# Optimization experiments

Measured on AMD Instinct MI355X. Metric: run time of the kernel, lower is better.

The kernel has to match this reference:

```python
import jax, jax.numpy as jnp
import numpy as np

NUM_GRAPHS = 256
NODES_PER_GRAPH = 64
K = 24
HID = 128

elu = jax.nn.elu


def _knn_edge_conv(x, Wc, bc):
    # x: [B*N, D]. Recompute kNN graph per graph, edge MLP, max-aggregate.
    B, N = NUM_GRAPHS, NODES_PER_GRAPH
    xg = x.reshape(B, N, -1)                       # [B, N, D]
    sq = jnp.sum(xg * xg, axis=-1)                 # [B, N]
    # squared euclidean distances within each graph: [B, N, N]
    d = sq[:, :, None] + sq[:, None, :] - 2.0 * jnp.einsum('bnd,bmd->bnm', xg, xg)
    _, idx = jax.lax.top_k(-d, K)                  # [B, N, K] nearest (incl. self)
    xj = jax.vmap(lambda g, i: g[i])(xg, idx)      # [B, N, K, D] neighbor gather
    xi = xg[:, :, None, :]                         # [B, N, 1, D]
    e = jnp.concatenate([jnp.broadcast_to(xi, xj.shape), xj - xi], axis=-1)  # [B,N,K,2D]
    m = elu(jnp.einsum('bnkf,fh->bnkh', e, Wc) + bc)
    out = jnp.max(m, axis=2)                       # max aggregation over K neighbors
    return out.reshape(B * N, -1)


def setup_inputs() -> dict:
    key = jax.random.key(0)
    ks = jax.random.split(key, 16)
    Ntot = NUM_GRAPHS * NODES_PER_GRAPH

    def w(k, fan_in, fan_out):
        return jax.random.normal(k, (fan_in, fan_out), jnp.float32) / np.sqrt(fan_in)

    return {
        'x_pf': jax.random.normal(ks[0], (Ntot, 15), jnp.float32),
        'batch_pf': jnp.repeat(jnp.arange(NUM_GRAPHS, dtype=jnp.int64 if jax.config.jax_enable_x64 else jnp.int32), NODES_PER_GRAPH),
        'W1': w(ks[1], 15, HID),  'b1': jnp.zeros((HID,), jnp.float32),
        'W2': w(ks[2], HID, HID), 'b2': jnp.zeros((HID,), jnp.float32),
        'Wc': w(ks[3], 2 * HID, HID), 'bc': jnp.zeros((HID,), jnp.float32),
        'Wo1': w(ks[4], HID, 64), 'bo1': jnp.zeros((64,), jnp.float32),
        'Wo2': w(ks[5], 64, 32),  'bo2': jnp.zeros((32,), jnp.float32),
        'Wo3': w(ks[6], 32, 32),  'bo3': jnp.zeros((32,), jnp.float32),
        'Wo4': w(ks[7], 32, 8),   'bo4': jnp.zeros((8,), jnp.float32),
    }


def reference(x_pf, batch_pf, W1, b1, W2, b2, Wc, bc, Wo1, bo1, Wo2, bo2, Wo3, bo3, Wo4, bo4):
    # pf_encode: Linear(15,128)+ELU+Linear(128,128)+ELU
    h = elu(elu(x_pf @ W1 + b1) @ W2 + b2)
    f1 = _knn_edge_conv(h, Wc, bc)
    f2 = _knn_edge_conv(f1, Wc, bc)
    f3 = _knn_edge_conv(f2, Wc, bc)
    # global_add_pool over nodes per graph
    pooled = jax.ops.segment_sum(f3, batch_pf, num_segments=NUM_GRAPHS)  # [B, 128]
    o = elu(pooled @ Wo1 + bo1)
    o = elu(o @ Wo2 + bo2)
    o = elu(o @ Wo3 + bo3)
    out = o @ Wo4 + bo4  # [B, 8]
    return (out, batch_pf)
```

## Files before the change

### kernel.cpp

```cpp
#include <hip/hip_runtime.h>
#include <hip/hip_bf16.h>
#include <math.h>

#define NG  256
#define NN  64
#define KK  24
#define HID 128
#define KP  136
#define FP  132
#define DP  68
#define FRAG 512
#define SLAB (8*4*2*FRAG)
#define HSLAB (8*4*FRAG)
#define IMG_BYTES (3*SLAB*2)

typedef __attribute__((ext_vector_type(8)))  short bf16x8;
typedef __attribute__((ext_vector_type(4)))  float f32x4;

__device__ __forceinline__ float elu1(float x){ return x > 0.f ? x : (expf(x)-1.f); }

__device__ __forceinline__ short bf_t(float x){ return (short)(__float_as_uint(x) >> 16); }
__device__ __forceinline__ float bf_u(short s){ return __uint_as_float(((unsigned)(unsigned short)s) << 16); }

extern "C" __global__ void prep_kernel(const float* __restrict__ W2,
                                       const float* __restrict__ Wc,
                                       short* __restrict__ img)
{
    int t = blockIdx.x * 256 + threadIdx.x;
    if (t >= 3*8*4*64) return;
    const int lane = t & 63;
    const int ks   = (t >> 6) & 3;
    const int tn   = (t >> 8) & 7;
    const int s    = t >> 11;
    const int n     = tn*16 + (lane & 15);
    const int kbase = ks*32 + (lane >> 4)*8;
    bf16x8 hv, lv;
    #pragma unroll
    for (int j = 0; j < 8; ++j){
        const int k = kbase + j;
        float w = (s == 0) ? W2[k*HID + n]
                : (s == 1) ? Wc[k*HID + n]
                           : Wc[(k + HID)*HID + n];
        short h = bf_t(w);
        hv[j] = h;
        lv[j] = bf_t(w - bf_u(h));
    }
    short* dst = img + s*SLAB + ((tn*4 + ks)*2)*FRAG + lane*8;
    *(bf16x8*)(dst)        = hv;
    *(bf16x8*)(dst + FRAG) = lv;
}

__device__ __forceinline__ void stage_copy(const short* __restrict__ src,
                                           short* __restrict__ slab, int tid)
{
    const uint4* s = (const uint4*)src;
    uint4* d = (uint4*)slab;
    #pragma unroll
    for (int i = 0; i < 4; ++i) d[tid + i*1024] = s[tid + i*1024];
}

__device__ __forceinline__ void stage_build(const float* __restrict__ Wg, int rowoff,
                                            short* __restrict__ slab, int tid)
{
    for (int i = tid; i < 8*4*64; i += 1024){
        const int lane2 = i & 63;
        const int ks    = (i >> 6) & 3;
        const int tn    = (i >> 8) & 7;
        const int n     = tn*16 + (lane2 & 15);
        const int kbase = ks*32 + (lane2 >> 4)*8;
        bf16x8 hv, lv;
        #pragma unroll
        for (int j = 0; j < 8; ++j){
            float w = Wg[(rowoff + kbase + j)*HID + n];
            short h = bf_t(w);
            hv[j] = h;
            lv[j] = bf_t(w - bf_u(h));
        }
        short* dst = slab + ((tn*4 + ks)*2)*FRAG + lane2*8;
        *(bf16x8*)(dst)        = hv;
        *(bf16x8*)(dst + FRAG) = lv;
    }
}

__device__ __forceinline__ void stage_hi_uv(const short* __restrict__ img,
                                            short* __restrict__ uv, int tid)
{
    const uint4* s = (const uint4*)img;
    uint4* d = (uint4*)uv;
    #pragma unroll
    for (int k = 0; k < 4; ++k){
        const int idx    = tid + k*1024;
        const int sl     = idx >> 11;
        const int within = idx & 2047;
        const int f      = within >> 6;
        const int w      = within & 63;
        d[idx] = s[(1 + sl)*4096 + f*128 + w];
    }
}

__device__ __forceinline__ void build_hi_uv(const float* __restrict__ Wc,
                                            short* __restrict__ uv, int tid)
{
    #pragma unroll
    for (int k = 0; k < 4; ++k){
        const int idx    = tid + k*1024;
        const int sl     = idx >> 11;
        const int within = idx & 2047;
        const int f      = within >> 6;
        const int lane2  = within & 63;
        const int tn = f >> 2, ks = f & 3;
        const int n     = tn*16 + (lane2 & 15);
        const int kbase = ks*32 + (lane2 >> 4)*8;
        const int rowoff = sl ? HID : 0;
        bf16x8 hv;
        #pragma unroll
        for (int j = 0; j < 8; ++j) hv[j] = bf_t(Wc[(rowoff + kbase + j)*HID + n]);
        *(bf16x8*)(uv + (size_t)idx*8) = hv;
    }
}

__device__ __forceinline__ void gemm16x2(const short* __restrict__ fbhi,
                                         const short* __restrict__ fblo,
                                         const short* __restrict__ slab,
                                         int tm, int tn0, int tn1, int lane,
                                         f32x4& c0, f32x4& c1)
{
    const int arow = tm*16 + (lane & 15);
    const int ko   = (lane >> 4) * 8;
    #pragma unroll 2
    for (int ks = 0; ks < 4; ++ks){
        bf16x8 ah = *(const bf16x8*)(fbhi + arow*KP + ks*32 + ko);
        bf16x8 al = *(const bf16x8*)(fblo + arow*KP + ks*32 + ko);
        const short* p0 = slab + ((tn0*4 + ks)*2)*FRAG + lane*8;
        const short* p1 = slab + ((tn1*4 + ks)*2)*FRAG + lane*8;
        bf16x8 bh0 = *(const bf16x8*)(p0);
        bf16x8 bl0 = *(const bf16x8*)(p0 + FRAG);
        bf16x8 bh1 = *(const bf16x8*)(p1);
        bf16x8 bl1 = *(const bf16x8*)(p1 + FRAG);
        c0 = __builtin_amdgcn_mfma_f32_16x16x32_bf16(ah, bh0, c0, 0,0,0);
        c0 = __builtin_amdgcn_mfma_f32_16x16x32_bf16(ah, bl0, c0, 0,0,0);
        c0 = __builtin_amdgcn_mfma_f32_16x16x32_bf16(al, bh0, c0, 0,0,0);
        c1 = __builtin_amdgcn_mfma_f32_16x16x32_bf16(ah, bh1, c1, 0,0,0);
        c1 = __builtin_amdgcn_mfma_f32_16x16x32_bf16(ah, bl1, c1, 0,0,0);
        c1 = __builtin_amdgcn_mfma_f32_16x16x32_bf16(al, bh1, c1, 0,0,0);
    }
}

__device__ __forceinline__ void gemm_uv(const short* __restrict__ fbhi,
                                        const short* __restrict__ fblo,
                                        const short* __restrict__ uhi,
                                        const short* __restrict__ vhi,
                                        int tm, int tn0, int tn1, int lane,
                                        f32x4& uA, f32x4& uB, f32x4& vA, f32x4& vB)
{
    const int arow = tm*16 + (lane & 15);
    const int ko   = (lane >> 4) * 8;
    #pragma unroll 2
    for (int ks = 0; ks < 4; ++ks){
        bf16x8 ah = *(const bf16x8*)(fbhi + arow*KP + ks*32 + ko);
        bf16x8 al = *(const bf16x8*)(fblo + arow*KP + ks*32 + ko);
        const int f0 = (tn0*4 + ks)*FRAG + lane*8;
        const int f1 = (tn1*4 + ks)*FRAG + lane*8;
        bf16x8 bu0 = *(const bf16x8*)(uhi + f0);
        bf16x8 bu1 = *(const bf16x8*)(uhi + f1);
        bf16x8 bv0 = *(const bf16x8*)(vhi + f0);
        bf16x8 bv1 = *(const bf16x8*)(vhi + f1);
        uA = __builtin_amdgcn_mfma_f32_16x16x32_bf16(ah, bu0, uA, 0,0,0);
        uA = __builtin_amdgcn_mfma_f32_16x16x32_bf16(al, bu0, uA, 0,0,0);
        uB = __builtin_amdgcn_mfma_f32_16x16x32_bf16(ah, bu1, uB, 0,0,0);
        uB = __builtin_amdgcn_mfma_f32_16x16x32_bf16(al, bu1, uB, 0,0,0);
        vA = __builtin_amdgcn_mfma_f32_16x16x32_bf16(ah, bv0, vA, 0,0,0);
        vA = __builtin_amdgcn_mfma_f32_16x16x32_bf16(al, bv0, vA, 0,0,0);
        vB = __builtin_amdgcn_mfma_f32_16x16x32_bf16(ah, bv1, vB, 0,0,0);
        vB = __builtin_amdgcn_mfma_f32_16x16x32_bf16(al, bv1, vB, 0,0,0);
    }
}

extern "C" __global__ void __launch_bounds__(1024)
dgcnn_kernel(const float* __restrict__ x_pf,
             const float* __restrict__ W1, const float* __restrict__ b1,
             const float* __restrict__ W2, const float* __restrict__ b2,
             const float* __restrict__ Wc, const float* __restrict__ bc,
             const float* __restrict__ Wo1, const float* __restrict__ bo1,
             const float* __restrict__ Wo2, const float* __restrict__ bo2,
             const float* __restrict__ Wo3, const float* __restrict__ bo3,
             const float* __restrict__ Wo4, const float* __restrict__ bo4,
             const short* __restrict__ img, int use_img,
             float* __restrict__ out)
{
    __shared__ __align__(16) short fbhi[NN*KP];
    __shared__ __align__(16) short fblo[NN*KP];
    __shared__ __align__(16) float dmt[NN*DP];
    __shared__ __align__(16) float Vbuf[NN*FP];
    __shared__ __align__(16) short wslab[SLAB];
    __shared__ int   knn[NN*KK];
    __shared__ float sq[NN];

    const int tid  = threadIdx.x;
    const int g    = blockIdx.x;
    const int lane = tid & 63;
    const int wv   = tid >> 6;
    const int row1 = tid >> 4;
    const int c0i  = (tid & 15) * 8;
    const int c2   = (tid & 15) * 4;

    const int t0  = wv*2, t1 = wv*2 + 1;
    const int gtm = t0 >> 3;
    const int gtn0 = t0 & 7, gtn1 = t1 & 7;

    if (tid < NN) out[NG*8 + g*NN + tid] = (float)g;

    if (use_img) stage_copy(img + 0*SLAB, wslab, tid); else stage_build(W2, 0, wslab, tid);

    {
        float acc[8];
        {
            float4 bA = *(const float4*)(b1 + c0i);
            float4 bB = *(const float4*)(b1 + c0i + 4);
            acc[0]=bA.x; acc[1]=bA.y; acc[2]=bA.z; acc[3]=bA.w;
            acc[4]=bB.x; acc[5]=bB.y; acc[6]=bB.z; acc[7]=bB.w;
        }
        #pragma unroll
        for (int f = 0; f < 15; ++f){
            float xv = x_pf[g*NN*15 + row1*15 + f];
            float4 wA = *(const float4*)(W1 + f*HID + c0i);
            float4 wB = *(const float4*)(W1 + f*HID + c0i + 4);
            acc[0] += xv*wA.x; acc[1] += xv*wA.y; acc[2] += xv*wA.z; acc[3] += xv*wA.w;
            acc[4] += xv*wB.x; acc[5] += xv*wB.y; acc[6] += xv*wB.z; acc[7] += xv*wB.w;
        }
        short4 hA, lA, hB, lB;
        float v;
        v = elu1(acc[0]); hA.x = bf_t(v); lA.x = bf_t(v - bf_u(hA.x));
        v = elu1(acc[1]); hA.y = bf_t(v); lA.y = bf_t(v - bf_u(hA.y));
        v = elu1(acc[2]); hA.z = bf_t(v); lA.z = bf_t(v - bf_u(hA.z));
        v = elu1(acc[3]); hA.w = bf_t(v); lA.w = bf_t(v - bf_u(hA.w));
        v = elu1(acc[4]); hB.x = bf_t(v); lB.x = bf_t(v - bf_u(hB.x));
        v = elu1(acc[5]); hB.y = bf_t(v); lB.y = bf_t(v - bf_u(hB.y));
        v = elu1(acc[6]); hB.z = bf_t(v); lB.z = bf_t(v - bf_u(hB.z));
        v = elu1(acc[7]); hB.w = bf_t(v); lB.w = bf_t(v - bf_u(hB.w));
        *(short4*)(fbhi + row1*KP + c0i)     = hA;
        *(short4*)(fbhi + row1*KP + c0i + 4) = hB;
        *(short4*)(fblo + row1*KP + c0i)     = lA;
        *(short4*)(fblo + row1*KP + c0i + 4) = lB;
    }
    __syncthreads();

    {
        f32x4 cA = {0,0,0,0}, cB = {0,0,0,0};
        gemm16x2(fbhi, fblo, wslab, gtm, gtn0, gtn1, lane, cA, cB);
        __syncthreads();
        #pragma unroll
        for (int half = 0; half < 2; ++half){
            const int tn  = half ? gtn1 : gtn0;
            const f32x4 c = half ? cB : cA;
            const int col = tn*16 + (lane & 15);
            const int rb  = gtm*16 + (lane >> 4)*4;
            const float bb = b2[col];
            #pragma unroll
            for (int e = 0; e < 4; ++e){
                float vv = elu1(c[e] + bb);
                short h = bf_t(vv);
                fbhi[(rb + e)*KP + col] = h;
                fblo[(rb + e)*KP + col] = bf_t(vv - bf_u(h));
            }
        }
        if (use_img) stage_hi_uv(img, wslab, tid); else build_hi_uv(Wc, wslab, tid);
    }
    __syncthreads();

    {
        bf16x8 hv = *(const bf16x8*)(fbhi + row1*KP + c0i);
        bf16x8 lv = *(const bf16x8*)(fblo + row1*KP + c0i);
        float s = 0.f;
        #pragma unroll
        for (int j = 0; j < 8; ++j){
            float vv = bf_u(hv[j]) + bf_u(lv[j]);
            s += vv*vv;
        }
        s += __shfl_xor(s, 1, 64);
        s += __shfl_xor(s, 2, 64);
        s += __shfl_xor(s, 4, 64);
        s += __shfl_xor(s, 8, 64);
        if ((tid & 15) == 0) sq[row1] = s;
    }
    __syncthreads();

    const short* Uhi = wslab;
    const short* Vhi = wslab + HSLAB;

    for (int layer = 0; layer < 3; ++layer){
        {
            f32x4 dc = {0.f, 0.f, 0.f, 0.f};
            const int tm0 = wv >> 2, tn0 = wv & 3;
            const int rA = tm0*16 + (lane & 15), rB = tn0*16 + (lane & 15);
            const int ko = (lane >> 4) * 8;
            #pragma unroll 2
            for (int ks = 0; ks < 4; ++ks){
                bf16x8 ah = *(const bf16x8*)(fbhi + rA*KP + ks*32 + ko);
                bf16x8 al = *(const bf16x8*)(fblo + rA*KP + ks*32 + ko);
                bf16x8 bh = *(const bf16x8*)(fbhi + rB*KP + ks*32 + ko);
                bf16x8 bl = *(const bf16x8*)(fblo + rB*KP + ks*32 + ko);
                dc = __builtin_amdgcn_mfma_f32_16x16x32_bf16(ah, bh, dc, 0,0,0);
                dc = __builtin_amdgcn_mfma_f32_16x16x32_bf16(ah, bl, dc, 0,0,0);
                dc = __builtin_amdgcn_mfma_f32_16x16x32_bf16(al, bh, dc, 0,0,0);
            }
            #pragma unroll
            for (int e = 0; e < 4; ++e){
                const int ra = tm0*16 + (lane >> 4)*4 + e, ca = tn0*16 + (lane & 15);
                dmt[ra*DP + ca] = sq[ra] + sq[ca] - 2.f*dc[e];
            }
        }
        __syncthreads();

        f32x4 uA = {0,0,0,0}, uB = {0,0,0,0}, vA = {0,0,0,0}, vB = {0,0,0,0};
        {
            #pragma unroll
            for (int p = 0; p < 4; ++p){
                const int r = wv*4 + p;
                const float dm = dmt[r*DP + lane];
                int rank = 0;
                #pragma unroll 4
                for (int q = 0; q < 16; ++q){
                    float4 v = *(const float4*)(dmt + r*DP + q*4);
                    rank += (v.x < dm) + (v.y < dm) + (v.z < dm) + (v.w < dm);
                }
                const unsigned long long mask = __ballot(rank < KK);
                if (rank < KK){
                    const int c = __popcll(mask & ((1ULL << lane) - 1ULL));
                    if (c < KK) knn[r*KK + c] = lane;
                }
            }
            __builtin_amdgcn_sched_barrier(0);
            gemm_uv(fbhi, fblo, Uhi, Vhi, gtm, gtn0, gtn1, lane, uA, uB, vA, vB);
        }
        __syncthreads();

        {
            #pragma unroll
            for (int half = 0; half < 2; ++half){
                const int tn  = half ? gtn1 : gtn0;
                const f32x4 cv = half ? vB : vA;
                const f32x4 cu = half ? uB : uA;
                const int col = tn*16 + (lane & 15);
                const int rb  = gtm*16 + (lane >> 4)*4;
                #pragma unroll
                for (int e = 0; e < 4; ++e){
                    Vbuf[(rb + e)*FP + col] = cv[e];
                    float u = cu[e];
                    short h = bf_t(u);
                    fbhi[(rb + e)*KP + col] = h;
                    fblo[(rb + e)*KP + col] = bf_t(u - bf_u(h));
                }
            }
        }
        __syncthreads();

        {
            float4 bcA = *(const float4*)(bc + c2);
            float4 bcB = *(const float4*)(bc + c2 + 64);
            float4 mxA = make_float4(-1e30f, -1e30f, -1e30f, -1e30f);
            float4 mxB = mxA;
            #pragma unroll 4
            for (int k = 0; k < KK; ++k){
                int j = knn[row1*KK + k];
                float4 va = *(const float4*)(Vbuf + j*FP + c2);
                float4 vb = *(const float4*)(Vbuf + j*FP + c2 + 64);
                mxA.x = fmaxf(mxA.x, va.x); mxA.y = fmaxf(mxA.y, va.y);
                mxA.z = fmaxf(mxA.z, va.z); mxA.w = fmaxf(mxA.w, va.w);
                mxB.x = fmaxf(mxB.x, vb.x); mxB.y = fmaxf(mxB.y, vb.y);
                mxB.z = fmaxf(mxB.z, vb.z); mxB.w = fmaxf(mxB.w, vb.w);
            }
            float4 vnA = *(const float4*)(Vbuf + row1*FP + c2);
            float4 vnB = *(const float4*)(Vbuf + row1*FP + c2 + 64);
            short4 uhA = *(const short4*)(fbhi + row1*KP + c2);
            short4 uhB = *(const short4*)(fbhi + row1*KP + c2 + 64);
            short4 ulA = *(const short4*)(fblo + row1*KP + c2);
            short4 ulB = *(const short4*)(fblo + row1*KP + c2 + 64);
            float o0 = elu1(bf_u(uhA.x) + bf_u(ulA.x) - vnA.x + bcA.x + mxA.x);
            float o1 = elu1(bf_u(uhA.y) + bf_u(ulA.y) - vnA.y + bcA.y + mxA.y);
            float o2 = elu1(bf_u(uhA.z) + bf_u(ulA.z) - vnA.z + bcA.z + mxA.z);
            float o3 = elu1(bf_u(uhA.w) + bf_u(ulA.w) - vnA.w + bcA.w + mxA.w);
            float o4 = elu1(bf_u(uhB.x) + bf_u(ulB.x) - vnB.x + bcB.x + mxB.x);
            float o5 = elu1(bf_u(uhB.y) + bf_u(ulB.y) - vnB.y + bcB.y + mxB.y);
            float o6 = elu1(bf_u(uhB.z) + bf_u(ulB.z) - vnB.z + bcB.z + mxB.z);
            float o7 = elu1(bf_u(uhB.w) + bf_u(ulB.w) - vnB.w + bcB.w + mxB.w);
            short4 nhA, nlA, nhB, nlB;
            nhA.x = bf_t(o0); nlA.x = bf_t(o0 - bf_u(nhA.x));
            nhA.y = bf_t(o1); nlA.y = bf_t(o1 - bf_u(nhA.y));
            nhA.z = bf_t(o2); nlA.z = bf_t(o2 - bf_u(nhA.z));
            nhA.w = bf_t(o3); nlA.w = bf_t(o3 - bf_u(nhA.w));
            nhB.x = bf_t(o4); nlB.x = bf_t(o4 - bf_u(nhB.x));
            nhB.y = bf_t(o5); nlB.y = bf_t(o5 - bf_u(nhB.y));
            nhB.z = bf_t(o6); nlB.z = bf_t(o6 - bf_u(nhB.z));
            nhB.w = bf_t(o7); nlB.w = bf_t(o7 - bf_u(nhB.w));
            *(short4*)(fbhi + row1*KP + c2)      = nhA;
            *(short4*)(fbhi + row1*KP + c2 + 64) = nhB;
            *(short4*)(fblo + row1*KP + c2)      = nlA;
            *(short4*)(fblo + row1*KP + c2 + 64) = nlB;
            float s = o0*o0 + o1*o1 + o2*o2 + o3*o3 + o4*o4 + o5*o5 + o6*o6 + o7*o7;
            s += __shfl_xor(s, 1, 64);
            s += __shfl_xor(s, 2, 64);
            s += __shfl_xor(s, 4, 64);
            s += __shfl_xor(s, 8, 64);
            if ((tid & 15) == 0) sq[row1] = s;
        }
        __syncthreads();
    }

    float* pooled = Vbuf;
    float* red    = Vbuf + 128;
    float* hr1    = Vbuf + 1152;
    float* hr2    = Vbuf + 1216;
    float* hr3    = Vbuf + 1248;

    {
        const int pq = tid >> 7, ch = tid & 127;
        float s = 0.f;
        for (int n = pq*8; n < pq*8 + 8; ++n)
            s += bf_u(fbhi[n*KP + ch]) + bf_u(fblo[n*KP + ch]);
        red[pq*HID + ch] = s;
    }
    __syncthreads();
    if (tid < HID){
        float s = 0.f;
        #pragma unroll
        for (int p = 0; p < 8; ++p) s += red[p*HID + tid];
        pooled[tid] = s;
    }
    __syncthreads();
    if (tid < 256){
        const int o = tid & 63, part = tid >> 6;
        float s = 0.f;
        for (int f = part*32; f < part*32 + 32; ++f) s += pooled[f] * Wo1[f*64 + o];
        red[part*64 + o] = s;
    }
    __syncthreads();
    if (tid < 64) hr1[tid] = elu1(bo1[tid] + red[tid] + red[64+tid] + red[128+tid] + red[192+tid]);
    __syncthreads();
    if (tid < 128){
        const int o = tid & 31, part = tid >> 5;
        float s = 0.f;
        for (int f = part*16; f < part*16 + 16; ++f) s += hr1[f] * Wo2[f*32 + o];
        red[part*32 + o] = s;
    }
    __syncthreads();
    if (tid < 32) hr2[tid] = elu1(bo2[tid] + red[tid] + red[32+tid] + red[64+tid] + red[96+tid]);
    __syncthreads();
    if (tid < 32){
        float a = bo3[tid];
        for (int f = 0; f < 32; ++f) a += hr2[f] * Wo3[f*32 + tid];
        hr3[tid] = elu1(a);
    }
    __syncthreads();
    if (tid < 8){
        float a = bo4[tid];
        for (int f = 0; f < 32; ++f) a += hr3[f] * Wo4[f*8 + tid];
        out[g*8 + tid] = a;
    }
}

extern "C" void kernel_launch(void* const* d_in, const int* in_sizes, int n_in,
                              void* d_out, int out_size, void* d_ws, size_t ws_size,
                              hipStream_t stream) {
    short* img = (short*)d_ws;
    const int use_img = (ws_size >= (size_t)IMG_BYTES) ? 1 : 0;
    if (use_img) {
        const int total = 3*8*4*64;
        prep_kernel<<<(total + 255)/256, 256, 0, stream>>>(
            (const float*)d_in[4], (const float*)d_in[6], img);
    }
    dgcnn_kernel<<<NG, 1024, 0, stream>>>(
        (const float*)d_in[0],
        (const float*)d_in[2],  (const float*)d_in[3],
        (const float*)d_in[4],  (const float*)d_in[5],
        (const float*)d_in[6],  (const float*)d_in[7],
        (const float*)d_in[8],  (const float*)d_in[9],
        (const float*)d_in[10], (const float*)d_in[11],
        (const float*)d_in[12], (const float*)d_in[13],
        (const float*)d_in[14], (const float*)d_in[15],
        img, use_img,
        (float*)d_out);
}
```

Measured before the change: 54.15 us.

## Fuse distance and U/V GEMMs into one phase, move kNN ranking after barrier

The U/V projection GEMM now runs in the same loop as the pairwise distance GEMM and reuses the same A fragments. The kNN rank selection moves into the phase that writes the U/V results back to shared memory. This removes one block-wide barrier per layer and avoids reloading the A operands. The neighbor indices are now read as int4 vectors, and the max-gather over all 24 neighbors is fully unrolled. The cost is more live accumulators during the fused loop, which raises register pressure under a 1024-thread launch bound.

```diff
diff --git a/kernel.cpp b/kernel.cpp
--- a/kernel.cpp
+++ b/kernel.cpp
@@ -146,36 +146,6 @@
     }
 }
 
-__device__ __forceinline__ void gemm_uv(const short* __restrict__ fbhi,
-                                        const short* __restrict__ fblo,
-                                        const short* __restrict__ uhi,
-                                        const short* __restrict__ vhi,
-                                        int tm, int tn0, int tn1, int lane,
-                                        f32x4& uA, f32x4& uB, f32x4& vA, f32x4& vB)
-{
-    const int arow = tm*16 + (lane & 15);
-    const int ko   = (lane >> 4) * 8;
-    #pragma unroll 2
-    for (int ks = 0; ks < 4; ++ks){
-        bf16x8 ah = *(const bf16x8*)(fbhi + arow*KP + ks*32 + ko);
-        bf16x8 al = *(const bf16x8*)(fblo + arow*KP + ks*32 + ko);
-        const int f0 = (tn0*4 + ks)*FRAG + lane*8;
-        const int f1 = (tn1*4 + ks)*FRAG + lane*8;
-        bf16x8 bu0 = *(const bf16x8*)(uhi + f0);
-        bf16x8 bu1 = *(const bf16x8*)(uhi + f1);
-        bf16x8 bv0 = *(const bf16x8*)(vhi + f0);
-        bf16x8 bv1 = *(const bf16x8*)(vhi + f1);
-        uA = __builtin_amdgcn_mfma_f32_16x16x32_bf16(ah, bu0, uA, 0,0,0);
-        uA = __builtin_amdgcn_mfma_f32_16x16x32_bf16(al, bu0, uA, 0,0,0);
-        uB = __builtin_amdgcn_mfma_f32_16x16x32_bf16(ah, bu1, uB, 0,0,0);
-        uB = __builtin_amdgcn_mfma_f32_16x16x32_bf16(al, bu1, uB, 0,0,0);
-        vA = __builtin_amdgcn_mfma_f32_16x16x32_bf16(ah, bv0, vA, 0,0,0);
-        vA = __builtin_amdgcn_mfma_f32_16x16x32_bf16(al, bv0, vA, 0,0,0);
-        vB = __builtin_amdgcn_mfma_f32_16x16x32_bf16(ah, bv1, vB, 0,0,0);
-        vB = __builtin_amdgcn_mfma_f32_16x16x32_bf16(al, bv1, vB, 0,0,0);
-    }
-}
-
 extern "C" __global__ void __launch_bounds__(1024)
 dgcnn_kernel(const float* __restrict__ x_pf,
              const float* __restrict__ W1, const float* __restrict__ b1,
@@ -289,49 +259,42 @@
     const short* Vhi = wslab + HSLAB;
 
     for (int layer = 0; layer < 3; ++layer){
+        f32x4 uA = {0,0,0,0}, uB = {0,0,0,0}, vA = {0,0,0,0}, vB = {0,0,0,0};
         {
             f32x4 dc = {0.f, 0.f, 0.f, 0.f};
-            const int tm0 = wv >> 2, tn0 = wv & 3;
-            const int rA = tm0*16 + (lane & 15), rB = tn0*16 + (lane & 15);
-            const int ko = (lane >> 4) * 8;
-            #pragma unroll 2
+            const int tm0 = wv >> 2, tn0d = wv & 3;
+            const int arow = tm0*16 + (lane & 15);
+            const int rB   = tn0d*16 + (lane & 15);
+            const int ko   = (lane >> 4) * 8;
+            #pragma unroll
             for (int ks = 0; ks < 4; ++ks){
-                bf16x8 ah = *(const bf16x8*)(fbhi + rA*KP + ks*32 + ko);
-                bf16x8 al = *(const bf16x8*)(fblo + rA*KP + ks*32 + ko);
+                bf16x8 ah = *(const bf16x8*)(fbhi + arow*KP + ks*32 + ko);
+                bf16x8 al = *(const bf16x8*)(fblo + arow*KP + ks*32 + ko);
                 bf16x8 bh = *(const bf16x8*)(fbhi + rB*KP + ks*32 + ko);
                 bf16x8 bl = *(const bf16x8*)(fblo + rB*KP + ks*32 + ko);
                 dc = __builtin_amdgcn_mfma_f32_16x16x32_bf16(ah, bh, dc, 0,0,0);
                 dc = __builtin_amdgcn_mfma_f32_16x16x32_bf16(ah, bl, dc, 0,0,0);
                 dc = __builtin_amdgcn_mfma_f32_16x16x32_bf16(al, bh, dc, 0,0,0);
+                const int f0 = (gtn0*4 + ks)*FRAG + lane*8;
+                const int f1 = (gtn1*4 + ks)*FRAG + lane*8;
+                bf16x8 bu0 = *(const bf16x8*)(Uhi + f0);
+                bf16x8 bu1 = *(const bf16x8*)(Uhi + f1);
+                bf16x8 bv0 = *(const bf16x8*)(Vhi + f0);
+                bf16x8 bv1 = *(const bf16x8*)(Vhi + f1);
+                uA = __builtin_amdgcn_mfma_f32_16x16x32_bf16(ah, bu0, uA, 0,0,0);
+                uA = __builtin_amdgcn_mfma_f32_16x16x32_bf16(al, bu0, uA, 0,0,0);
+                uB = __builtin_amdgcn_mfma_f32_16x16x32_bf16(ah, bu1, uB, 0,0,0);
+                uB = __builtin_amdgcn_mfma_f32_16x16x32_bf16(al, bu1, uB, 0,0,0);
+                vA = __builtin_amdgcn_mfma_f32_16x16x32_bf16(ah, bv0, vA, 0,0,0);
+                vA = __builtin_amdgcn_mfma_f32_16x16x32_bf16(al, bv0, vA, 0,0,0);
+                vB = __builtin_amdgcn_mfma_f32_16x16x32_bf16(ah, bv1, vB, 0,0,0);
+                vB = __builtin_amdgcn_mfma_f32_16x16x32_bf16(al, bv1, vB, 0,0,0);
             }
             #pragma unroll
             for (int e = 0; e < 4; ++e){
-                const int ra = tm0*16 + (lane >> 4)*4 + e, ca = tn0*16 + (lane & 15);
+                const int ra = tm0*16 + (lane >> 4)*4 + e, ca = tn0d*16 + (lane & 15);
                 dmt[ra*DP + ca] = sq[ra] + sq[ca] - 2.f*dc[e];
             }
-        }
-        __syncthreads();
-
-        f32x4 uA = {0,0,0,0}, uB = {0,0,0,0}, vA = {0,0,0,0}, vB = {0,0,0,0};
-        {
-            #pragma unroll
-            for (int p = 0; p < 4; ++p){
-                const int r = wv*4 + p;
-                const float dm = dmt[r*DP + lane];
-                int rank = 0;
-                #pragma unroll 4
-                for (int q = 0; q < 16; ++q){
-                    float4 v = *(const float4*)(dmt + r*DP + q*4);
-                    rank += (v.x < dm) + (v.y < dm) + (v.z < dm) + (v.w < dm);
-                }
-                const unsigned long long mask = __ballot(rank < KK);
-                if (rank < KK){
-                    const int c = __popcll(mask & ((1ULL << lane) - 1ULL));
-                    if (c < KK) knn[r*KK + c] = lane;
-                }
-            }
-            __builtin_amdgcn_sched_barrier(0);
-            gemm_uv(fbhi, fblo, Uhi, Vhi, gtm, gtn0, gtn1, lane, uA, uB, vA, vB);
         }
         __syncthreads();
 
@@ -352,24 +315,51 @@
                     fblo[(rb + e)*KP + col] = bf_t(u - bf_u(h));
                 }
             }
+            #pragma unroll
+            for (int p = 0; p < 4; ++p){
+                const int r = wv*4 + p;
+                const float dm = dmt[r*DP + lane];
+                int rank = 0;
+                #pragma unroll 4
+                for (int q = 0; q < 16; ++q){
+                    float4 v = *(const float4*)(dmt + r*DP + q*4);
+                    rank += (v.x < dm) + (v.y < dm) + (v.z < dm) + (v.w < dm);
+                }
+                const unsigned long long mask = __ballot(rank < KK);
+                if (rank < KK){
+                    const int c = __popcll(mask & ((1ULL << lane) - 1ULL));
+                    if (c < KK) knn[r*KK + c] = lane;
+                }
+            }
         }
         __syncthreads();
 
         {
+            const int* kr = knn + row1*KK;
+            int4 j0 = *(const int4*)(kr);
+            int4 j1 = *(const int4*)(kr + 4);
+            int4 j2 = *(const int4*)(kr + 8);
+            int4 j3 = *(const int4*)(kr + 12);
+            int4 j4 = *(const int4*)(kr + 16);
+            int4 j5 = *(const int4*)(kr + 20);
+            float4 mxA = make_float4(-1e30f, -1e30f, -1e30f, -1e30f);
+            float4 mxB = mxA;
+            #define GM(J) { \
+                float4 va = *(const float4*)(Vbuf + (J)*FP + c2); \
+                float4 vb = *(const float4*)(Vbuf + (J)*FP + c2 + 64); \
+                mxA.x = fmaxf(mxA.x, va.x); mxA.y = fmaxf(mxA.y, va.y); \
+                mxA.z = fmaxf(mxA.z, va.z); mxA.w = fmaxf(mxA.w, va.w); \
+                mxB.x = fmaxf(mxB.x, vb.x); mxB.y = fmaxf(mxB.y, vb.y); \
+                mxB.z = fmaxf(mxB.z, vb.z); mxB.w = fmaxf(mxB.w, vb.w); }
+            GM(j0.x) GM(j0.y) GM(j0.z) GM(j0.w)
+            GM(j1.x) GM(j1.y) GM(j1.z) GM(j1.w)
+            GM(j2.x) GM(j2.y) GM(j2.z) GM(j2.w)
+            GM(j3.x) GM(j3.y) GM(j3.z) GM(j3.w)
+            GM(j4.x) GM(j4.y) GM(j4.z) GM(j4.w)
+            GM(j5.x) GM(j5.y) GM(j5.z) GM(j5.w)
+            #undef GM
             float4 bcA = *(const float4*)(bc + c2);
             float4 bcB = *(const float4*)(bc + c2 + 64);
-            float4 mxA = make_float4(-1e30f, -1e30f, -1e30f, -1e30f);
-            float4 mxB = mxA;
-            #pragma unroll 4
-            for (int k = 0; k < KK; ++k){
-                int j = knn[row1*KK + k];
-                float4 va = *(const float4*)(Vbuf + j*FP + c2);
-                float4 vb = *(const float4*)(Vbuf + j*FP + c2 + 64);
-                mxA.x = fmaxf(mxA.x, va.x); mxA.y = fmaxf(mxA.y, va.y);
-                mxA.z = fmaxf(mxA.z, va.z); mxA.w = fmaxf(mxA.w, va.w);
-                mxB.x = fmaxf(mxB.x, vb.x); mxB.y = fmaxf(mxB.y, vb.y);
-                mxB.z = fmaxf(mxB.z, vb.z); mxB.w = fmaxf(mxB.w, vb.w);
-            }
             float4 vnA = *(const float4*)(Vbuf + row1*FP + c2);
             float4 vnB = *(const float4*)(Vbuf + row1*FP + c2 + 64);
             short4 uhA = *(const short4*)(fbhi + row1*KP + c2);
```

Result: faster. 52.51 us (-3.0%).
